# Optimization experiments

Hardware: AMD Instinct MI355X
Metric: run time of the kernel (lower is better)

Reference implementation:

```python
import jax, jax.numpy as jnp
import numpy as np


def setup_inputs() -> dict:
    B, K, E, M, H, T, V = 32, 64, 512, 512, 512, 20, 32000
    key = jax.random.key(0)
    ks = jax.random.split(key, 8)
    s = 0.02
    return {
        "encoder_outputs": jax.random.normal(ks[0], (B, K, E), jnp.float32),
        "embedding_table": jax.random.normal(ks[1], (V, M), jnp.float32) * s,
        "Wa": jax.random.normal(ks[2], (2 * H + E, 1), jnp.float32) * s,
        "ba": jnp.zeros((1,), jnp.float32),
        "W_ih": jax.random.normal(ks[3], (4 * H, E + M), jnp.float32) * s,
        "W_hh": jax.random.normal(ks[4], (4 * H, H), jnp.float32) * s,
        "b_ih": jnp.zeros((4 * H,), jnp.float32),
        "b_hh": jnp.zeros((4 * H,), jnp.float32),
        "Wl": jax.random.normal(ks[5], (V, 2 * H + E + M), jnp.float32) * s,
        "bl": jnp.zeros((V,), jnp.float32),
        "captions": jax.random.randint(ks[6], (B, T), 0, V),
        "use_teacher_forcing": 1,
    }


def reference(encoder_outputs, embedding_table, Wa, ba, W_ih, W_hh, b_ih, b_hh,
              Wl, bl, captions, use_teacher_forcing):
    B, K, E = encoder_outputs.shape
    H = W_hh.shape[1]
    tf = bool(use_teacher_forcing)  # static python flag

    # h0 = c0 = last encoder output (requires E == H, as in the source)
    h0 = encoder_outputs[:, -1, :]
    c0 = h0

    caps_seq = captions.T  # (T, B); captions[:, i] becomes next token after step i

    def step(carry, cap_t):
        h, c, token = carry
        emb = embedding_table[token]                       # (B, M), dropout=0
        flat_state = jnp.concatenate([h, c], axis=-1)      # (B, 2H)
        # Bahdanau alignment over all K encoder steps at once
        al_in = jnp.concatenate(
            [jnp.broadcast_to(flat_state[:, None, :], (B, K, 2 * H)),
             encoder_outputs], axis=-1)                    # (B, K, 2H+E)
        scores = jnp.tanh(al_in @ Wa + ba)[..., 0]         # (B, K)
        attn = jax.nn.softmax(scores, axis=1)
        context = jnp.einsum('bk,bke->be', attn, encoder_outputs)  # (B, E)
        x = jnp.concatenate([context, emb], axis=-1)       # (B, E+M) == rnn_input
        # single LSTM step, PyTorch gate order i,f,g,o
        gates = x @ W_ih.T + b_ih + h @ W_hh.T + b_hh
        i_g, f_g, g_g, o_g = jnp.split(gates, 4, axis=-1)
        c_new = jax.nn.sigmoid(f_g) * c + jax.nn.sigmoid(i_g) * jnp.tanh(g_g)
        h_new = jax.nn.sigmoid(o_g) * jnp.tanh(c_new)
        # NOTE: source concatenates the PRE-update state here (faithful)
        final_input = jnp.concatenate([flat_state, x], axis=-1)  # (B, 2H+E+M)
        logp = jax.nn.log_softmax(final_input @ Wl.T + bl, axis=1)  # (B, V)
        next_token = cap_t if tf else jnp.argmax(logp, axis=1)
        return (h_new, c_new, next_token), logp

    init = (h0, c0, captions[:, 0])
    _, probs = jax.lax.scan(step, init, caps_seq)
    return jnp.transpose(probs, (1, 0, 2))  # (B, T, V)
```

## Files before the change

### kernel.cpp

```cpp
#include <hip/hip_runtime.h>
#include <hip/hip_bf16.h>
#include <stdint.h>

#define B_   32
#define K_   64
#define E_   512
#define H_   512
#define M_   512
#define T_   20
#define V_   32000
#define KIN  2048
#define NBLK 32

typedef __bf16 bf16x8 __attribute__((ext_vector_type(8)));
typedef float  f32x4  __attribute__((ext_vector_type(4)));

__device__ inline unsigned short f2bf_rne(float f) {
  union { float f; unsigned u; } v; v.f = f;
  unsigned r = v.u + 0x7FFFu + ((v.u >> 16) & 1u);
  return (unsigned short)(r >> 16);
}
__device__ inline float bf2f(unsigned short s) {
  union { unsigned u; float f; } v; v.u = ((unsigned)s) << 16;
  return v.f;
}
__device__ inline float sigm(float x) { return 1.f / (1.f + expf(-x)); }
__device__ inline unsigned ordf(float f) {
  unsigned u = __float_as_uint(f);
  return (u & 0x80000000u) ? ~u : (u | 0x80000000u);
}
__device__ __forceinline__ void gload16(const void* g, void* l) {
  __builtin_amdgcn_global_load_lds(
      (const __attribute__((address_space(1))) void*)g,
      (__attribute__((address_space(3))) void*)l, 16, 0, 0);
}


__global__ void k_prep(const float* __restrict__ W_ih, const float* __restrict__ W_hh,
                       const float* __restrict__ b_ih, const float* __restrict__ b_hh,
                       const float* __restrict__ enc, const float* __restrict__ embt,
                       const int* __restrict__ captions,
                       unsigned short* __restrict__ wih_hi, unsigned short* __restrict__ wih_lo,
                       unsigned short* __restrict__ whh_hi, unsigned short* __restrict__ whh_lo,
                       unsigned short* __restrict__ enc_bf, unsigned short* __restrict__ emb_bf,
                       float* __restrict__ bias_arr, float* __restrict__ score_part,
                       unsigned long long* __restrict__ argkey,
                       const float* __restrict__ Wl, unsigned short* __restrict__ wl_bf,
                       unsigned short* __restrict__ Fall) {
  int tid0 = blockIdx.x * 256 + threadIdx.x;
  int NT = gridDim.x * 256;
  for (int i = tid0; i < V_ * KIN / 4; i += NT) {
    f32x4 v = __builtin_nontemporal_load((const f32x4*)Wl + i);
    ushort4 o;
    o.x = f2bf_rne(v.x); o.y = f2bf_rne(v.y); o.z = f2bf_rne(v.z); o.w = f2bf_rne(v.w);
    ((ushort4*)wl_bf)[i] = o;
  }
  for (int i = tid0; i < 2048 * 1024; i += NT) {
    float f = W_ih[i];
    unsigned short h = f2bf_rne(f);
    wih_hi[i] = h; wih_lo[i] = f2bf_rne(f - bf2f(h));
  }
  for (int i = tid0; i < NBLK * 64 * 512; i += NT) {
    int e = i & 511, jj = (i >> 9) & 63, blk = i >> 15;
    int jg = (jj >> 4) * 512 + blk * 16 + (jj & 15);
    float f = W_hh[jg * 512 + e];
    unsigned short h = f2bf_rne(f);
    whh_hi[i] = h; whh_lo[i] = f2bf_rne(f - bf2f(h));
  }
  for (int i = tid0; i < 2048 * 512; i += NT) enc_bf[i] = f2bf_rne(enc[i]);
  for (int i = tid0; i < 640 * 512; i += NT) {
    int n = i >> 9, m = i & 511;
    int t = n >> 5, b = n & 31;
    int tok = captions[b * T_ + (t > 0 ? t - 1 : 0)];
    unsigned short ev = f2bf_rne(embt[(size_t)tok * 512 + m]);
    emb_bf[i] = ev;
    Fall[(size_t)n * KIN + 1536 + m] = ev;
  }
  for (int i = tid0; i < 2048; i += NT) {
    int blk = i >> 6, jj = i & 63;
    int jg = (jj >> 4) * 512 + blk * 16 + (jj & 15);
    bias_arr[i] = b_ih[jg] + b_hh[jg];
  }
  for (int i = tid0; i < (T_ + 1) * 1024; i += NT) score_part[i] = 0.f;
  for (int i = tid0; i < 32; i += NT) argkey[i] = 0ull;
}

__global__ void k_init(const float* __restrict__ enc, const float* __restrict__ Wa,
                       float* __restrict__ hb, float* __restrict__ cb,
                       unsigned short* __restrict__ Fall,
                       float* __restrict__ enc_score, float* __restrict__ score_part) {
  int idx = blockIdx.x * 256 + threadIdx.x;
  int b = idx >> 9, i = idx & 511;
  float v = enc[(size_t)b * K_ * E_ + (size_t)(K_ - 1) * E_ + i];
  hb[b * H_ + i] = v;
  cb[b * H_ + i] = v;
  unsigned short bv = f2bf_rne(v);
  Fall[b * KIN + i] = bv;
  Fall[b * KIN + H_ + i] = bv;
  if (idx < B_ * K_) {
    int bb = idx >> 6, k = idx & 63;
    const float4* e4  = (const float4*)(enc + ((size_t)bb * K_ + k) * E_);
    const float4* wa4 = (const float4*)(Wa + 2 * H_);
    float acc = 0.f;
    #pragma unroll 4
    for (int q = 0; q < E_ / 4; ++q) {
      float4 a = e4[q], w = wa4[q];
      acc += a.x * w.x + a.y * w.y + a.z * w.z + a.w * w.w;
    }
    enc_score[idx] = acc;
  }
  if (idx < 2048) {
    int bb = idx >> 6, l = idx & 63;
    float s = 0.f;
    #pragma unroll
    for (int q = 0; q < 8; ++q) {
      int ii = l * 8 + q;
      float hv = enc[(size_t)bb * K_ * E_ + (size_t)(K_ - 1) * E_ + ii];
      s += hv * (Wa[ii] + Wa[512 + ii]);
    }
    for (int o = 32; o; o >>= 1) s += __shfl_down(s, o);
    if (l == 0) score_part[bb] = s;
  }
}

__global__ __launch_bounds__(256) void k_gpre(
    const unsigned short* __restrict__ whi, const unsigned short* __restrict__ wlo,
    int koff, const unsigned short* __restrict__ Bm,
    float* __restrict__ outp, int N) {
  int blk = blockIdx.x, nt = blockIdx.y;
  int tid = threadIdx.x;
  int l = tid & 63, w = tid >> 6, lv = l & 15, lg = l >> 4;
  const int n0 = nt * 128 + w * 32;

  f32x4 acc[4][2];
  #pragma unroll
  for (int jf = 0; jf < 4; ++jf)
    #pragma unroll
    for (int nf = 0; nf < 2; ++nf) acc[jf][nf] = (f32x4){0.f, 0.f, 0.f, 0.f};

  #pragma unroll 4
  for (int kk = 0; kk < 16; ++kk) {
    bf16x8 bfr[2];
    #pragma unroll
    for (int nf = 0; nf < 2; ++nf)
      bfr[nf] = *(const bf16x8*)(Bm + (size_t)(n0 + nf * 16 + lv) * 512 + kk * 32 + lg * 8);
    #pragma unroll
    for (int jf = 0; jf < 4; ++jf) {
      int jg = jf * 512 + blk * 16 + lv;
      bf16x8 ahi = *(const bf16x8*)(whi + (size_t)jg * 1024 + koff + kk * 32 + lg * 8);
      bf16x8 alo = *(const bf16x8*)(wlo + (size_t)jg * 1024 + koff + kk * 32 + lg * 8);
      #pragma unroll
      for (int nf = 0; nf < 2; ++nf) {
        acc[jf][nf] = __builtin_amdgcn_mfma_f32_16x16x32_bf16(ahi, bfr[nf], acc[jf][nf], 0, 0, 0);
        acc[jf][nf] = __builtin_amdgcn_mfma_f32_16x16x32_bf16(alo, bfr[nf], acc[jf][nf], 0, 0, 0);
      }
    }
  }
  #pragma unroll
  for (int jf = 0; jf < 4; ++jf)
    #pragma unroll
    for (int nf = 0; nf < 2; ++nf)
      #pragma unroll
      for (int jr = 0; jr < 4; ++jr) {
        int n = n0 + nf * 16 + lv;
        int jj = jf * 16 + 4 * lg + jr;
        outp[((size_t)blk * N + n) * 64 + jj] = acc[jf][nf][jr];
      }
}

__global__ __launch_bounds__(512) void k_step(
    const float* __restrict__ enc, const float* __restrict__ embt,
    const float* __restrict__ Wa, const float* __restrict__ ba,
    const float* __restrict__ W_ih, const float* __restrict__ W_hh,
    const float* __restrict__ b_ih, const float* __restrict__ b_hh,
    const float* __restrict__ Wl, const float* __restrict__ bl,
    const int* __restrict__ captions, const int* __restrict__ tf_flag,
    const float* __restrict__ Genc, const float* __restrict__ Gemb,
    const unsigned short* __restrict__ whh_hi, const unsigned short* __restrict__ whh_lo,
    const float* __restrict__ bias_arr, const float* __restrict__ enc_score,
    float* __restrict__ score_part, unsigned short* __restrict__ Fall,
    float* __restrict__ hb, float* __restrict__ cb,
    unsigned long long* __restrict__ argkey, int t) {
  const int blk = blockIdx.x;
  const int tid = threadIdx.x;
  __shared__ float attn_s[B_ * K_];
  __shared__ float gsA[64 * 33];
  __shared__ float gsH[2][64][32];
  __shared__ float scC[512];
  __shared__ float score_t_[32];
  __shared__ int   token_sp;
  __shared__ float xls[KIN];
  __shared__ float gls[2048];
  __shared__ unsigned long long bred[512];
  const float* cbc = cb + (t & 1) * B_ * H_;
  float* cbn = cb + ((t + 1) & 1) * B_ * H_;

  if (tf_flag[0]) {
    if (tid < 32) {
      float s = 0.f;
      #pragma unroll 8
      for (int p = 0; p < 32; ++p) s += score_part[t * 1024 + p * 32 + tid];
      score_t_[tid] = s;
    }
    __syncthreads();
    {
      int w = tid >> 6, l = tid & 63;
      float ba0 = ba[0];
      #pragma unroll
      for (int bb = 0; bb < 4; ++bb) {
        int b = w * 4 + bb;
        float s = tanhf(score_t_[b] + enc_score[b * 64 + l] + ba0);
        float m = s;
        for (int o = 32; o; o >>= 1) m = fmaxf(m, __shfl_xor(m, o));
        float e = expf(s - m);
        float sum = e;
        for (int o = 32; o; o >>= 1) sum += __shfl_xor(sum, o);
        attn_s[b * 64 + l] = e / sum;
      }
    }
    __syncthreads();
    {
      const f32x4* G4 = (const f32x4*)Genc;
      const f32x4* E4 = (const f32x4*)Gemb;
      const f32x4* B4 = (const f32x4*)bias_arr;
      int b = tid >> 4, jj4 = tid & 15;
      const f32x4* gp = G4 + ((size_t)blk * 2048 + b * 64) * 16 + jj4;
      const float* ap = attn_s + b * 64;
      f32x4 s = {0.f, 0.f, 0.f, 0.f};
      #pragma unroll 8
      for (int k = 0; k < 64; ++k) {
        float a = ap[k];
        f32x4 g = gp[(size_t)k * 16];
        s[0] += a * g[0]; s[1] += a * g[1]; s[2] += a * g[2]; s[3] += a * g[3];
      }
      f32x4 e = E4[((size_t)blk * 640 + t * 32 + b) * 16 + jj4];
      f32x4 bb = B4[blk * 16 + jj4];
      #pragma unroll
      for (int q = 0; q < 4; ++q) {
        float v = s[q] + (e[q] + bb[q]);
        gsA[(jj4 * 4 + q) * 33 + b] = v;
      }
    }
    {
      const float* aw = attn_s + blk * 64;
      int e = tid;
      if (e < 512) {
        float a = 0.f;
        #pragma unroll 8
        for (int k = 0; k < 64; ++k) a += aw[k] * enc[((size_t)blk * 64 + k) * 512 + e];
        Fall[((size_t)t * 32 + blk) * KIN + 1024 + e] = f2bf_rne(a);
      }
    }
    {
      int w = tid >> 6, l = tid & 63, lv = l & 15, lg = l >> 4;
      int g = w & 3, h2 = w >> 2;
      const unsigned short* ah = whh_hi + ((size_t)blk * 64 + g * 16 + lv) * 512 + h2 * 256 + lg * 8;
      const unsigned short* al = whh_lo + ((size_t)blk * 64 + g * 16 + lv) * 512 + h2 * 256 + lg * 8;
      const unsigned short* f0 = Fall + ((size_t)t * 32 + lv) * KIN + h2 * 256 + lg * 8;
      const unsigned short* f1 = Fall + ((size_t)t * 32 + 16 + lv) * KIN + h2 * 256 + lg * 8;
      f32x4 a0 = {0.f, 0.f, 0.f, 0.f};
      f32x4 a1 = {0.f, 0.f, 0.f, 0.f};
      #pragma unroll 8
      for (int kk = 0; kk < 8; ++kk) {
        bf16x8 hi = *(const bf16x8*)(ah + kk * 32);
        bf16x8 lo = *(const bf16x8*)(al + kk * 32);
        bf16x8 b0 = *(const bf16x8*)(f0 + kk * 32);
        bf16x8 b1 = *(const bf16x8*)(f1 + kk * 32);
        a0 = __builtin_amdgcn_mfma_f32_16x16x32_bf16(hi, b0, a0, 0, 0, 0);
        a0 = __builtin_amdgcn_mfma_f32_16x16x32_bf16(lo, b0, a0, 0, 0, 0);
        a1 = __builtin_amdgcn_mfma_f32_16x16x32_bf16(hi, b1, a1, 0, 0, 0);
        a1 = __builtin_amdgcn_mfma_f32_16x16x32_bf16(lo, b1, a1, 0, 0, 0);
      }
      #pragma unroll
      for (int jr = 0; jr < 4; ++jr) {
        int jj = g * 16 + 4 * lg + jr;
        gsH[h2][jj][lv]      = a0[jr];
        gsH[h2][jj][16 + lv] = a1[jr];
      }
    }
    __syncthreads();
    {
      int b = tid & 31, r = tid >> 5;
      int ii = blk * 16 + r;
      float ig = gsA[(r) * 33 + b]      + gsH[0][r][b]      + gsH[1][r][b];
      float fg = gsA[(16 + r) * 33 + b] + gsH[0][16 + r][b] + gsH[1][16 + r][b];
      float gg = gsA[(32 + r) * 33 + b] + gsH[0][32 + r][b] + gsH[1][32 + r][b];
      float og = gsA[(48 + r) * 33 + b] + gsH[0][48 + r][b] + gsH[1][48 + r][b];
      float cv = cbc[b * H_ + ii];
      float cn = sigm(fg) * cv + sigm(ig) * tanhf(gg);
      float hn = sigm(og) * tanhf(cn);
      cbn[b * H_ + ii] = cn;
      Fall[((size_t)(t + 1) * 32 + b) * KIN + ii] = f2bf_rne(hn);
      Fall[((size_t)(t + 1) * 32 + b) * KIN + H_ + ii] = f2bf_rne(cn);
      scC[r * 32 + b] = hn * Wa[ii] + cn * Wa[512 + ii];
    }
    __syncthreads();
    if (tid < 32) {
      float s = 0.f;
      #pragma unroll
      for (int r = 0; r < 16; ++r) s += scC[r * 32 + tid];
      score_part[(t + 1) * 1024 + blk * 32 + tid] = s;
    }
  } else {
    const int b = blk;
    const float* hbc = hb + (t & 1) * B_ * H_;
    float* hbn = hb + ((t + 1) & 1) * B_ * H_;
    if (tid == 0) {
      float s = 0.f;
      for (int p = 0; p < 32; ++p) s += score_part[t * 1024 + p * 32 + b];
      score_t_[0] = s;
      token_sp = (t == 0) ? captions[b * T_]
                          : (int)(0xFFFFFFFFu - (unsigned)(argkey[b] & 0xFFFFFFFFull));
    }
    __syncthreads();
    if (tid < 64) {
      float s = tanhf(score_t_[0] + enc_score[b * 64 + tid] + ba[0]);
      float m = s;
      for (int o = 32; o; o >>= 1) m = fmaxf(m, __shfl_xor(m, o));
      float e = expf(s - m);
      float sum = e;
      for (int o = 32; o; o >>= 1) sum += __shfl_xor(sum, o);
      attn_s[tid] = e / sum;
    }
    __syncthreads();
    for (int i = tid; i < 512; i += 512) {
      xls[i] = hbc[b * H_ + i];
      xls[512 + i] = cbc[b * H_ + i];
      float a = 0.f;
      for (int k = 0; k < 64; ++k) a += attn_s[k] * enc[((size_t)b * 64 + k) * 512 + i];
      xls[1024 + i] = a;
      xls[1536 + i] = embt[(size_t)token_sp * 512 + i];
    }
    __syncthreads();
    for (int i = tid; i < 1024; i += 512)
      Fall[((size_t)t * 32 + b) * KIN + 1024 + i] = f2bf_rne(xls[1024 + i]);
    for (int j = tid; j < 2048; j += 512) {
      float a = b_ih[j] + b_hh[j];
      for (int e = 0; e < 1024; ++e) a += W_ih[(size_t)j * 1024 + e] * xls[1024 + e];
      for (int e = 0; e < 512; ++e)  a += W_hh[(size_t)j * 512 + e] * xls[e];
      gls[j] = a;
    }
    __syncthreads();
    {
      float sc = 0.f;
      for (int i = tid; i < 512; i += 512) {
        float ig = gls[i], fg = gls[512 + i], gg = gls[1024 + i], og = gls[1536 + i];
        float cv = xls[512 + i];
        float cn = sigm(fg) * cv + sigm(ig) * tanhf(gg);
        float hn = sigm(og) * tanhf(cn);
        hbn[b * H_ + i] = hn;
        cbn[b * H_ + i] = cn;
        Fall[((size_t)(t + 1) * 32 + b) * KIN + i] = f2bf_rne(hn);
        Fall[((size_t)(t + 1) * 32 + b) * KIN + H_ + i] = f2bf_rne(cn);
        sc += hn * Wa[i] + cn * Wa[512 + i];
      }
      scC[tid] = sc;
    }
    __syncthreads();
    if (tid == 0) {
      float s = 0.f;
      for (int q = 0; q < 512; ++q) s += scC[q];
      score_part[(t + 1) * 1024 + b] = s;
    }
    unsigned long long best = 0ull;
    for (int v = tid; v < V_; v += 512) {
      float d = bl[v];
      const float* wr = Wl + (size_t)v * KIN;
      for (int k = 0; k < KIN; ++k) d += wr[k] * xls[k];
      unsigned long long key = ((unsigned long long)ordf(d) << 32) | (0xFFFFFFFFu - (unsigned)v);
      if (key > best) best = key;
    }
    bred[tid] = best;
    __syncthreads();
    for (int o = 256; o; o >>= 1) {
      if (tid < o) bred[tid] = bred[tid] > bred[tid + o] ? bred[tid] : bred[tid + o];
      __syncthreads();
    }
    if (tid == 0) argkey[b] = bred[0];
  }
}

#define GM   128
#define GNP  320
#define ABYTES 40960
#define BUFB  57344

__global__ __launch_bounds__(512, 2) void k_gemm(
    const unsigned short* __restrict__ wl_bf,
    const unsigned short* __restrict__ F,
    const float* __restrict__ bl,
    float* __restrict__ out) {
  extern __shared__ unsigned char lds[];
  const int tid = threadIdx.x;
  const int l = tid & 63, w = tid >> 6, lv = l & 15, lg = l >> 4;
  const int wm = w >> 2, wn = w & 3;
  const int m0 = blockIdx.x * GM;

  float blv[4];
  #pragma unroll
  for (int mi = 0; mi < 4; ++mi) blv[mi] = bl[m0 + wm * 64 + mi * 16 + lv];

  f32x4 acc[4][5];
  #pragma unroll
  for (int mi = 0; mi < 4; ++mi)
    #pragma unroll
    for (int ni = 0; ni < 5; ++ni) acc[mi][ni] = (f32x4){0.f, 0.f, 0.f, 0.f};

#define STAGE(c, buf) do {                                                    \
    int kb_ = ((c) & 31) * 64;                                                \
    int nb_ = ((c) >> 5) * GNP;                                               \
    unsigned char* bs_ = lds + (buf) * BUFB;                                  \
    _Pragma("unroll")                                                         \
    for (int i_ = 0; i_ < 5; ++i_) {                                          \
      int s_ = i_ * 512 + tid;                                                \
      int kq_ = s_ / 320, n_ = s_ - kq_ * 320;                                \
      gload16(F + (size_t)(nb_ + n_) * KIN + kb_ + kq_ * 8, bs_ + s_ * 16);   \
    }                                                                         \
    _Pragma("unroll")                                                         \
    for (int j_ = 0; j_ < 2; ++j_) {                                          \
      int s_ = j_ * 512 + tid;                                                \
      int kq_ = s_ >> 7, m_ = s_ & 127;                                       \
      gload16(wl_bf + (size_t)(m0 + m_) * KIN + kb_ + kq_ * 8,                \
              bs_ + ABYTES + s_ * 16);                                        \
    }                                                                         \
  } while (0)

#define COMPUTE(buf) do {                                                     \
    unsigned char* bs_ = lds + (buf) * BUFB;                                  \
    _Pragma("unroll")                                                         \
    for (int kk2_ = 0; kk2_ < 2; ++kk2_) {                                    \
      int kq_ = kk2_ * 4 + lg;                                                \
      bf16x8 bf_[4];                                                          \
      _Pragma("unroll")                                                       \
      for (int mi = 0; mi < 4; ++mi)                                          \
        bf_[mi] = *(const bf16x8*)(bs_ + ABYTES +                             \
                    (size_t)(kq_ * 128 + wm * 64 + mi * 16 + lv) * 16);       \
      _Pragma("unroll")                                                       \
      for (int ni = 0; ni < 5; ++ni) {                                        \
        bf16x8 af_ = *(const bf16x8*)(bs_ +                                   \
                    (size_t)(kq_ * 320 + wn * 80 + ni * 16 + lv) * 16);       \
        _Pragma("unroll")                                                     \
        for (int mi = 0; mi < 4; ++mi)                                        \
          acc[mi][ni] = __builtin_amdgcn_mfma_f32_16x16x32_bf16(              \
                          af_, bf_[mi], acc[mi][ni], 0, 0, 0);                \
      }                                                                       \
    }                                                                         \
  } while (0)

#define WRITEOUT(pass) do {                                                   \
    _Pragma("unroll")                                                         \
    for (int mi = 0; mi < 4; ++mi) {                                          \
      int v_ = m0 + wm * 64 + mi * 16 + lv;                                   \
      _Pragma("unroll")                                                       \
      for (int ni = 0; ni < 5; ++ni) {                                        \
        _Pragma("unroll")                                                     \
        for (int j_ = 0; j_ < 4; ++j_) {                                      \
          int n_ = (pass) * GNP + wn * 80 + ni * 16 + 4 * lg + j_;            \
          int tt_ = n_ >> 5, bb_ = n_ & 31;                                   \
          out[((size_t)bb_ * T_ + tt_) * V_ + v_] = acc[mi][ni][j_] + blv[mi];\
        }                                                                     \
      }                                                                       \
    }                                                                         \
  } while (0)

  STAGE(0, 0);
  int cur = 0;
  for (int c = 0; c < 64; ++c) {
    __syncthreads();
    if (c < 63) STAGE(c + 1, cur ^ 1);
    COMPUTE(cur);
    if (c == 31) {
      WRITEOUT(0);
      #pragma unroll
      for (int mi = 0; mi < 4; ++mi)
        #pragma unroll
        for (int ni = 0; ni < 5; ++ni) acc[mi][ni] = (f32x4){0.f, 0.f, 0.f, 0.f};
    }
    cur ^= 1;
  }
  WRITEOUT(1);
#undef STAGE
#undef COMPUTE
#undef WRITEOUT
}

__global__ void k_lsm(float* __restrict__ out) {
  float4* p = (float4*)(out + (size_t)blockIdx.x * V_);
  int tid = threadIdx.x;
  __shared__ float smax[4], ssum[4];
  const int N4 = V_ / 4;
  float m = -1e30f, s = 0.f;
  for (int i = tid; i < N4; i += 256) {
    float4 v = p[i];
    float lm = fmaxf(fmaxf(v.x, v.y), fmaxf(v.z, v.w));
    if (lm > m) { s *= expf(m - lm); m = lm; }
    s += expf(v.x - m) + expf(v.y - m) + expf(v.z - m) + expf(v.w - m);
  }
  for (int o = 32; o; o >>= 1) {
    float m2 = __shfl_xor(m, o), s2 = __shfl_xor(s, o);
    float mn = fmaxf(m, m2);
    s = s * expf(m - mn) + s2 * expf(m2 - mn);
    m = mn;
  }
  if ((tid & 63) == 0) { smax[tid >> 6] = m; ssum[tid >> 6] = s; }
  __syncthreads();
  float mg = fmaxf(fmaxf(smax[0], smax[1]), fmaxf(smax[2], smax[3]));
  float sg = ssum[0] * expf(smax[0] - mg) + ssum[1] * expf(smax[1] - mg)
           + ssum[2] * expf(smax[2] - mg) + ssum[3] * expf(smax[3] - mg);
  float lse = mg + logf(sg);
  for (int i = tid; i < N4; i += 256) {
    float4 v = p[i];
    v.x -= lse; v.y -= lse; v.z -= lse; v.w -= lse;
    p[i] = v;
  }
}

extern "C" void kernel_launch(void* const* d_in, const int* in_sizes, int n_in,
                              void* d_out, int out_size, void* d_ws, size_t ws_size,
                              hipStream_t stream) {
  const float* enc      = (const float*)d_in[0];
  const float* embt     = (const float*)d_in[1];
  const float* Wa       = (const float*)d_in[2];
  const float* ba       = (const float*)d_in[3];
  const float* W_ih     = (const float*)d_in[4];
  const float* W_hh     = (const float*)d_in[5];
  const float* b_ih     = (const float*)d_in[6];
  const float* b_hh     = (const float*)d_in[7];
  const float* Wl       = (const float*)d_in[8];
  const float* bl       = (const float*)d_in[9];
  const int*   captions = (const int*)d_in[10];
  const int*   tf       = (const int*)d_in[11];
  float* out = (float*)d_out;
  char*  ws  = (char*)d_ws;

  size_t off = 0;
  unsigned short* Fall = (unsigned short*)(ws + off); off += (size_t)(T_ + 1) * B_ * KIN * 2;
  float* hb            = (float*)(ws + off);          off += (size_t)2 * B_ * H_ * 4;
  float* cb            = (float*)(ws + off);          off += (size_t)2 * B_ * H_ * 4;
  float* enc_score     = (float*)(ws + off);          off += (size_t)B_ * K_ * 4;
  float* score_part    = (float*)(ws + off);          off += (size_t)(T_ + 1) * 1024 * 4;
  unsigned long long* argkey = (unsigned long long*)(ws + off); off += 256;
  float* bias_arr      = (float*)(ws + off);          off += 2048 * 4;
  off = (off + 1023) & ~(size_t)1023;
  unsigned short* wih_hi = (unsigned short*)(ws + off); off += (size_t)2048 * 1024 * 2;
  unsigned short* wih_lo = (unsigned short*)(ws + off); off += (size_t)2048 * 1024 * 2;
  unsigned short* whh_hi = (unsigned short*)(ws + off); off += (size_t)NBLK * 64 * 512 * 2;
  unsigned short* whh_lo = (unsigned short*)(ws + off); off += (size_t)NBLK * 64 * 512 * 2;
  unsigned short* enc_bf = (unsigned short*)(ws + off); off += (size_t)2048 * 512 * 2;
  unsigned short* emb_bf = (unsigned short*)(ws + off); off += (size_t)640 * 512 * 2;
  float* Genc          = (float*)(ws + off);          off += (size_t)NBLK * 2048 * 64 * 4;
  float* Gemb          = (float*)(ws + off);          off += (size_t)NBLK * 640 * 64 * 4;
  unsigned short* wl_bf = (unsigned short*)(ws + off); off += (size_t)V_ * KIN * 2;

  k_prep<<<512, 256, 0, stream>>>(W_ih, W_hh, b_ih, b_hh, enc, embt, captions,
                                  wih_hi, wih_lo, whh_hi, whh_lo, enc_bf, emb_bf,
                                  bias_arr, score_part, argkey, Wl, wl_bf, Fall);
  k_init<<<64, 256, 0, stream>>>(enc, Wa, hb, cb, Fall, enc_score, score_part);
  k_gpre<<<dim3(NBLK, 16), 256, 0, stream>>>(wih_hi, wih_lo, 0, enc_bf, Genc, 2048);
  k_gpre<<<dim3(NBLK, 5), 256, 0, stream>>>(wih_hi, wih_lo, 512, emb_bf, Gemb, 640);

  for (int t = 0; t < T_; ++t) {
    k_step<<<NBLK, 512, 0, stream>>>(enc, embt, Wa, ba, W_ih, W_hh, b_ih, b_hh,
                                     Wl, bl, captions, tf, Genc, Gemb,
                                     whh_hi, whh_lo, bias_arr, enc_score,
                                     score_part, Fall, hb, cb, argkey, t);
  }
  k_gemm<<<V_ / GM, 512, 2 * BUFB, stream>>>(wl_bf, Fall, bl, out);
  k_lsm<<<B_ * T_, 256, 0, stream>>>(out);
}
```

Before: 807.3 us.

## Overlap Wl bf16 conversion with recurrent steps and retile output GEMM

Moves the fp32-to-bf16 conversion of the large output projection weight out of the prep kernel and into extra blocks of each sequential step launch. Each of the 20 step launches converts one slice, so the conversion runs on CUs the 32-block recurrence leaves idle. The output GEMM is also retiled to 64 rows per block, stages only the weight tile in LDS, and reads the activation fragments straight from global memory, which gives twice as many blocks. Reading activations directly from global memory may add latency and repeated traffic, and the extra blocks could slow the latency-critical step kernel.

```diff
diff --git a/kernel.cpp b/kernel.cpp
--- a/kernel.cpp
+++ b/kernel.cpp
@@ -11,6 +11,7 @@
 #define V_   32000
 #define KIN  2048
 #define NBLK 32
+#define NCONV 224
 
 typedef __bf16 bf16x8 __attribute__((ext_vector_type(8)));
 typedef float  f32x4  __attribute__((ext_vector_type(4)));
@@ -45,16 +46,9 @@
                        unsigned short* __restrict__ enc_bf, unsigned short* __restrict__ emb_bf,
                        float* __restrict__ bias_arr, float* __restrict__ score_part,
                        unsigned long long* __restrict__ argkey,
-                       const float* __restrict__ Wl, unsigned short* __restrict__ wl_bf,
                        unsigned short* __restrict__ Fall) {
   int tid0 = blockIdx.x * 256 + threadIdx.x;
   int NT = gridDim.x * 256;
-  for (int i = tid0; i < V_ * KIN / 4; i += NT) {
-    f32x4 v = __builtin_nontemporal_load((const f32x4*)Wl + i);
-    ushort4 o;
-    o.x = f2bf_rne(v.x); o.y = f2bf_rne(v.y); o.z = f2bf_rne(v.z); o.w = f2bf_rne(v.w);
-    ((ushort4*)wl_bf)[i] = o;
-  }
   for (int i = tid0; i < 2048 * 1024; i += NT) {
     float f = W_ih[i];
     unsigned short h = f2bf_rne(f);
@@ -180,9 +174,25 @@
     const float* __restrict__ bias_arr, const float* __restrict__ enc_score,
     float* __restrict__ score_part, unsigned short* __restrict__ Fall,
     float* __restrict__ hb, float* __restrict__ cb,
-    unsigned long long* __restrict__ argkey, int t) {
+    unsigned long long* __restrict__ argkey, unsigned short* __restrict__ wl_bf,
+    int t) {
   const int blk = blockIdx.x;
   const int tid = threadIdx.x;
+
+  if (blk >= NBLK) {
+    const int NC = V_ * KIN / 4;
+    const int per = (NC + T_ - 1) / T_;
+    int lo = t * per;
+    int hi = lo + per; if (hi > NC) hi = NC;
+    for (int i = lo + (blk - NBLK) * 512 + tid; i < hi; i += NCONV * 512) {
+      f32x4 v = __builtin_nontemporal_load((const f32x4*)Wl + i);
+      ushort4 o;
+      o.x = f2bf_rne(v.x); o.y = f2bf_rne(v.y); o.z = f2bf_rne(v.z); o.w = f2bf_rne(v.w);
+      ((ushort4*)wl_bf)[i] = o;
+    }
+    return;
+  }
+
   __shared__ float attn_s[B_ * K_];
   __shared__ float gsA[64 * 33];
   __shared__ float gsH[2][64][32];
@@ -380,10 +390,9 @@
   }
 }
 
-#define GM   128
+#define GM   64
 #define GNP  320
-#define ABYTES 40960
-#define BUFB  57344
+#define BUFB 8192
 
 __global__ __launch_bounds__(512, 2) void k_gemm(
     const unsigned short* __restrict__ wl_bf,
@@ -396,51 +405,42 @@
   const int wm = w >> 2, wn = w & 3;
   const int m0 = blockIdx.x * GM;
 
-  float blv[4];
+  float blv[2];
   #pragma unroll
-  for (int mi = 0; mi < 4; ++mi) blv[mi] = bl[m0 + wm * 64 + mi * 16 + lv];
-
-  f32x4 acc[4][5];
+  for (int mi = 0; mi < 2; ++mi) blv[mi] = bl[m0 + wm * 32 + mi * 16 + lv];
+
+  f32x4 acc[2][5];
   #pragma unroll
-  for (int mi = 0; mi < 4; ++mi)
+  for (int mi = 0; mi < 2; ++mi)
     #pragma unroll
     for (int ni = 0; ni < 5; ++ni) acc[mi][ni] = (f32x4){0.f, 0.f, 0.f, 0.f};
 
 #define STAGE(c, buf) do {                                                    \
+    int kb_ = ((c) & 31) * 64;                                                \
+    unsigned char* bs_ = lds + (buf) * BUFB;                                  \
+    int kq_ = tid >> 6, m_ = tid & 63;                                        \
+    gload16(wl_bf + (size_t)(m0 + m_) * KIN + kb_ + kq_ * 8, bs_ + tid * 16); \
+  } while (0)
+
+#define COMPUTE(c, buf) do {                                                  \
     int kb_ = ((c) & 31) * 64;                                                \
     int nb_ = ((c) >> 5) * GNP;                                               \
     unsigned char* bs_ = lds + (buf) * BUFB;                                  \
     _Pragma("unroll")                                                         \
-    for (int i_ = 0; i_ < 5; ++i_) {                                          \
-      int s_ = i_ * 512 + tid;                                                \
-      int kq_ = s_ / 320, n_ = s_ - kq_ * 320;                                \
-      gload16(F + (size_t)(nb_ + n_) * KIN + kb_ + kq_ * 8, bs_ + s_ * 16);   \
-    }                                                                         \
-    _Pragma("unroll")                                                         \
-    for (int j_ = 0; j_ < 2; ++j_) {                                          \
-      int s_ = j_ * 512 + tid;                                                \
-      int kq_ = s_ >> 7, m_ = s_ & 127;                                       \
-      gload16(wl_bf + (size_t)(m0 + m_) * KIN + kb_ + kq_ * 8,                \
-              bs_ + ABYTES + s_ * 16);                                        \
-    }                                                                         \
-  } while (0)
-
-#define COMPUTE(buf) do {                                                     \
-    unsigned char* bs_ = lds + (buf) * BUFB;                                  \
-    _Pragma("unroll")                                                         \
     for (int kk2_ = 0; kk2_ < 2; ++kk2_) {                                    \
       int kq_ = kk2_ * 4 + lg;                                                \
-      bf16x8 bf_[4];                                                          \
+      bf16x8 bf_[2];                                                          \
       _Pragma("unroll")                                                       \
-      for (int mi = 0; mi < 4; ++mi)                                          \
-        bf_[mi] = *(const bf16x8*)(bs_ + ABYTES +                             \
-                    (size_t)(kq_ * 128 + wm * 64 + mi * 16 + lv) * 16);       \
+      for (int mi = 0; mi < 2; ++mi)                                          \
+        bf_[mi] = *(const bf16x8*)(bs_ +                                      \
+                    (size_t)(kq_ * 64 + wm * 32 + mi * 16 + lv) * 16);        \
       _Pragma("unroll")                                                       \
       for (int ni = 0; ni < 5; ++ni) {                                        \
-        bf16x8 af_ = *(const bf16x8*)(bs_ +                                   \
-                    (size_t)(kq_ * 320 + wn * 80 + ni * 16 + lv) * 16);       \
+        bf16x8 af_ = *(const bf16x8*)(F +                                     \
+                    (size_t)(nb_ + wn * 80 + ni * 16 + lv) * KIN +            \
+                    kb_ + kq_ * 8);                                           \
         _Pragma("unroll")                                                     \
-        for (int mi = 0; mi < 4; ++mi)                                        \
+        for (int mi = 0; mi < 2; ++mi)                                        \
           acc[mi][ni] = __builtin_amdgcn_mfma_f32_16x16x32_bf16(              \
                           af_, bf_[mi], acc[mi][ni], 0, 0, 0);                \
       }                                                                       \
@@ -449,8 +449,8 @@
 
 #define WRITEOUT(pass) do {                                                   \
     _Pragma("unroll")                                                         \
-    for (int mi = 0; mi < 4; ++mi) {                                          \
-      int v_ = m0 + wm * 64 + mi * 16 + lv;                                   \
+    for (int mi = 0; mi < 2; ++mi) {                                          \
+      int v_ = m0 + wm * 32 + mi * 16 + lv;                                   \
       _Pragma("unroll")                                                       \
       for (int ni = 0; ni < 5; ++ni) {                                        \
         _Pragma("unroll")                                                     \
@@ -468,11 +468,11 @@
   for (int c = 0; c < 64; ++c) {
     __syncthreads();
     if (c < 63) STAGE(c + 1, cur ^ 1);
-    COMPUTE(cur);
+    COMPUTE(c, cur);
     if (c == 31) {
       WRITEOUT(0);
       #pragma unroll
-      for (int mi = 0; mi < 4; ++mi)
+      for (int mi = 0; mi < 2; ++mi)
         #pragma unroll
         for (int ni = 0; ni < 5; ++ni) acc[mi][ni] = (f32x4){0.f, 0.f, 0.f, 0.f};
     }
@@ -554,16 +554,17 @@
 
   k_prep<<<512, 256, 0, stream>>>(W_ih, W_hh, b_ih, b_hh, enc, embt, captions,
                                   wih_hi, wih_lo, whh_hi, whh_lo, enc_bf, emb_bf,
-                                  bias_arr, score_part, argkey, Wl, wl_bf, Fall);
+                                  bias_arr, score_part, argkey, Fall);
   k_init<<<64, 256, 0, stream>>>(enc, Wa, hb, cb, Fall, enc_score, score_part);
   k_gpre<<<dim3(NBLK, 16), 256, 0, stream>>>(wih_hi, wih_lo, 0, enc_bf, Genc, 2048);
   k_gpre<<<dim3(NBLK, 5), 256, 0, stream>>>(wih_hi, wih_lo, 512, emb_bf, Gemb, 640);
 
   for (int t = 0; t < T_; ++t) {
-    k_step<<<NBLK, 512, 0, stream>>>(enc, embt, Wa, ba, W_ih, W_hh, b_ih, b_hh,
-                                     Wl, bl, captions, tf, Genc, Gemb,
-                                     whh_hi, whh_lo, bias_arr, enc_score,
-                                     score_part, Fall, hb, cb, argkey, t);
+    k_step<<<NBLK + NCONV, 512, 0, stream>>>(
+        enc, embt, Wa, ba, W_ih, W_hh, b_ih, b_hh,
+        Wl, bl, captions, tf, Genc, Gemb,
+        whh_hi, whh_lo, bias_arr, enc_score,
+        score_part, Fall, hb, cb, argkey, wl_bf, t);
   }
   k_gemm<<<V_ / GM, 512, 2 * BUFB, stream>>>(wl_bf, Fall, bl, out);
   k_lsm<<<B_ * T_, 256, 0, stream>>>(out);
```

Result: slower. 926.8 us (+14.8%).
